# Optimization experiments

Measured on AMD Instinct MI355X. Metric: run time of the kernel, lower is better.

Reference implementation:

```python
import jax, jax.numpy as jnp
import numpy as np

B, S, D, H = 8, 2048, 1024, 8
CHUNK = D // H
SCALE = float(D) ** (-0.5)  # key_dim ** -0.5, key_dim == num_units here
LN_EPS = 1e-5


def setup_inputs() -> dict:
    key = jax.random.key(0)
    ks = jax.random.split(key, 9)
    s = 0.02
    return {
        "query": jax.random.normal(ks[0], (B, S, D), jnp.float32),
        "keys": jax.random.normal(ks[1], (B, S, D), jnp.float32),
        "Wq": jax.random.normal(ks[2], (D, D), jnp.float32) * s,  # torch Linear weight [out,in]
        "Wk": jax.random.normal(ks[3], (D, D), jnp.float32) * s,
        "Wv": jax.random.normal(ks[4], (D, D), jnp.float32) * s,
        "Wp": jax.random.normal(ks[5], (D, D), jnp.float32) * s,
        "bp": jnp.zeros((D,), jnp.float32),
        "ln_gamma": jnp.ones((D,), jnp.float32),
        "ln_beta": jnp.zeros((D,), jnp.float32),
    }


def reference(query, keys, Wq, Wk, Wv, Wp, bp, ln_gamma, ln_beta):
    # Linear layers (no bias on q/k/v): y = x @ W.T
    Q = jnp.einsum("bsd,ed->bse", query, Wq)
    K = jnp.einsum("bsd,ed->bse", keys, Wk)
    V = jnp.einsum("bsd,ed->bse", keys, Wv)
    # Faithful to original: raw view to [B*h, S, chunk] (no transpose head split)
    Qh = Q.reshape(B * H, S, CHUNK)
    Kh = K.reshape(B * H, S, CHUNK)
    Vh = V.reshape(B * H, S, CHUNK)
    # scores [B*h, S, S], scale, softmax (is_masked=False, dropout_p=0)
    att = jnp.einsum("gqc,gkc->gqk", Qh, Kh) * SCALE
    att = jax.nn.softmax(att, axis=-1)
    ctx = jnp.einsum("gqk,gkc->gqc", att, Vh).reshape(B, S, D)
    # output projection + residual + LayerNorm
    out = jnp.einsum("bsd,ed->bse", ctx, Wp) + bp
    out = out + query
    mu = jnp.mean(out, axis=-1, keepdims=True)
    var = jnp.mean(jnp.square(out - mu), axis=-1, keepdims=True)
    out = (out - mu) * jax.lax.rsqrt(var + LN_EPS) * ln_gamma + ln_beta
    return out
```

## Files before the change

kernel.cpp:

```cpp
#include <hip/hip_runtime.h>

typedef __bf16 bf16x8 __attribute__((ext_vector_type(8)));
typedef float f32x4 __attribute__((ext_vector_type(4)));

#define SCLOG 0.04508422f

__device__ __forceinline__ unsigned short f2bf(float f) {
  union { float f; unsigned int u; } v;
  v.f = f;
  unsigned int u = v.u;
  u += 0x7fffu + ((u >> 16) & 1u);
  return (unsigned short)(u >> 16);
}

__device__ __forceinline__ void gld_lds16(const void* g, void* l) {
  __builtin_amdgcn_global_load_lds(
      (const __attribute__((address_space(1))) void*)g,
      (__attribute__((address_space(3))) void*)l, 16, 0, 0);
}

__global__ __launch_bounds__(256) void convert_kernel(
    const float* __restrict__ q, const float* __restrict__ k,
    const float* __restrict__ wq, const float* __restrict__ wk,
    const float* __restrict__ wv, const float* __restrict__ wp,
    unsigned short* __restrict__ qb, unsigned short* __restrict__ kb,
    unsigned short* __restrict__ Wqkv, unsigned short* __restrict__ Wpb) {
  size_t i = (size_t)blockIdx.x * 256 + threadIdx.x;
  const float* src; unsigned short* dst; size_t off;
  if (i < 4194304)      { src = q;  dst = qb;             off = i; }
  else if (i < 8388608) { src = k;  dst = kb;             off = i - 4194304; }
  else if (i < 8650752) { src = wq; dst = Wqkv;           off = i - 8388608; }
  else if (i < 8912896) { src = wk; dst = Wqkv + 1048576; off = i - 8650752; }
  else if (i < 9175040) { src = wv; dst = Wqkv + 2097152; off = i - 8912896; }
  else                  { src = wp; dst = Wpb;            off = i - 9175040; }
  float4 v = ((const float4*)src)[off];
  ushort4 o;
  o.x = f2bf(v.x); o.y = f2bf(v.y); o.z = f2bf(v.z); o.w = f2bf(v.w);
  ((ushort4*)dst)[off] = o;
}

#define QKV_BAR __builtin_amdgcn_s_barrier()
#define QKV_LGKM asm volatile("s_waitcnt lgkmcnt(0)" ::: "memory")

#define QKV_STG(lc, h, srcb, s)                                               \
  gld_lds16((srcb) + (size_t)(s) * 128 + gro0, (lc) + (h) * 16384 + d0);      \
  gld_lds16((srcb) + (size_t)(s) * 128 + gro1, (lc) + (h) * 16384 + d0 + 1024);

#define QKV_RDA(I0)                                                           \
  _Pragma("unroll") for (int i4 = 0; i4 < 4; ++i4) {                          \
    af[i4][0] = *(const bf16x8*)(tb + rbA + ((I0) + i4) * 2048 + cx0);        \
    af[i4][1] = *(const bf16x8*)(tb + rbA + ((I0) + i4) * 2048 + cx1);        \
  }

#define QKV_RDB(JP)                                                           \
  _Pragma("unroll") for (int j2 = 0; j2 < 2; ++j2) {                          \
    bfr[JP][j2][0] = *(const bf16x8*)(tb + rbB + ((JP) * 2 + j2) * 2048 + cx0); \
    bfr[JP][j2][1] = *(const bf16x8*)(tb + rbB + ((JP) * 2 + j2) * 2048 + cx1); \
  }

#define QKV_MM(I0, JP)                                                        \
  _Pragma("unroll") for (int i4 = 0; i4 < 4; ++i4)                            \
  _Pragma("unroll") for (int j2 = 0; j2 < 2; ++j2)                            \
  _Pragma("unroll") for (int kk = 0; kk < 2; ++kk)                            \
    acc[(I0) + i4][(JP) * 2 + j2] = __builtin_amdgcn_mfma_f32_16x16x32_bf16(  \
        af[i4][kk], bfr[JP][j2][kk], acc[(I0) + i4][(JP) * 2 + j2], 0, 0, 0);

__global__ __launch_bounds__(512, 2) void gemm_qkv8_kernel(
    const unsigned short* __restrict__ qb,
    const unsigned short* __restrict__ kb,
    const unsigned short* __restrict__ W,
    unsigned short* __restrict__ Qo,
    unsigned short* __restrict__ Ko,
    unsigned short* __restrict__ Vo) {
  __shared__ char lds[131072];

  const int t = threadIdx.x;
  const int lane = t & 63;
  const int w = t >> 6;
  const int fr = lane & 15;
  const int quad = lane >> 4;

  const int orig = blockIdx.x;
  const int sseq = orig >> 3;
  const int tn = sseq >> 3;
  const int tm = (orig & 7) * 8 + (sseq & 7);

  const unsigned short* Ap = (tn < 4) ? qb : kb;
  const char* aBase = (const char*)Ap + (size_t)(tm * 256) * 2048;
  const char* bBase = (const char*)W + (size_t)(tn * 256) * 2048;

  const int wm2 = w >> 2, wn4 = w & 3;

  const size_t gro0 = (size_t)(w * 16 + (lane >> 3)) * 2048 + (size_t)(((lane & 7) ^ (lane >> 3)) << 4);
  const size_t gro1 = gro0 + 8 * 2048;
  const int d0 = w * 2048 + lane * 16;

  const int rbA = (wm2 * 128 + fr) * 128;
  const int rbB = 32768 + (wn4 * 64 + fr) * 128;
  const int cx0 = (quad * 16) ^ ((fr & 7) << 4);
  const int cx1 = cx0 ^ 64;

  f32x4 acc[8][4];
#pragma unroll
  for (int i = 0; i < 8; ++i)
#pragma unroll
    for (int j = 0; j < 4; ++j) acc[i][j] = (f32x4){0.f, 0.f, 0.f, 0.f};

#pragma unroll
  for (int s = 0; s < 2; ++s) {
    char* lc = lds + s * 65536;
    QKV_STG(lc, 0, aBase, s);
    QKV_STG(lc, 1, aBase + 262144, s);
    QKV_STG(lc + 32768, 0, bBase, s);
    QKV_STG(lc + 32768, 1, bBase + 262144, s);
  }
  asm volatile("s_waitcnt vmcnt(8)" ::: "memory");
  QKV_BAR;

#pragma unroll 1
  for (int kt = 0; kt < 16; ++kt) {
    const char* tb = lds + (kt & 1) * 65536;
    char* lc = lds + (kt & 1) * 65536;
    const int s = kt + 2;
    bf16x8 af[4][2], bfr[2][2][2];

    QKV_RDA(0);
    QKV_RDB(0);
    QKV_BAR; QKV_LGKM;
    __builtin_amdgcn_s_setprio(1);
    QKV_MM(0, 0);
    __builtin_amdgcn_s_setprio(0);
    QKV_BAR;

    QKV_RDB(1);
    QKV_BAR; QKV_LGKM;
    __builtin_amdgcn_s_setprio(1);
    QKV_MM(0, 1);
    __builtin_amdgcn_s_setprio(0);
    QKV_BAR;

    QKV_RDA(4);
    if (s < 16) {
      QKV_STG(lc + 32768, 0, bBase, s);
      QKV_STG(lc + 32768, 1, bBase + 262144, s);
    }
    QKV_BAR; QKV_LGKM;
    __builtin_amdgcn_s_setprio(1);
    QKV_MM(4, 1);
    __builtin_amdgcn_s_setprio(0);
    QKV_BAR;

    if (s < 16) {
      QKV_STG(lc, 0, aBase, s);
      QKV_STG(lc, 1, aBase + 262144, s);
    }
    QKV_BAR;
    __builtin_amdgcn_s_setprio(1);
    QKV_MM(4, 0);
    __builtin_amdgcn_s_setprio(0);
    if (kt <= 13)      { asm volatile("s_waitcnt vmcnt(8)" ::: "memory"); }
    else if (kt == 14) { asm volatile("s_waitcnt vmcnt(0)" ::: "memory"); }
    if (kt < 15) QKV_BAR;
  }

  const int sel = tn >> 2;
  unsigned short* Out = sel == 0 ? Qo : (sel == 1 ? Ko : Vo);
  const float osc = (sel == 0) ? SCLOG : 1.f;
  const int row0 = tm * 256 + wm2 * 128 + quad * 4;
  const int col0 = (tn & 3) * 256 + wn4 * 64 + fr;
#pragma unroll
  for (int i = 0; i < 8; ++i)
#pragma unroll
    for (int j = 0; j < 4; ++j)
#pragma unroll
      for (int r = 0; r < 4; ++r)
        Out[(size_t)(row0 + i * 16 + r) * 1024 + col0 + j * 16] = f2bf(acc[i][j][r] * osc);
}

__global__ __launch_bounds__(256) void vtrans_kernel(
    const unsigned short* __restrict__ V, unsigned short* __restrict__ Vt) {
  __shared__ unsigned short T[128 * 136];
  const int g  = blockIdx.x >> 4;
  const int kt = blockIdx.x & 15;
  const unsigned short* Vg = V + (size_t)g * 262144 + (size_t)kt * 128 * 128;
  unsigned short* Vtg = Vt + (size_t)g * 262144 + kt * 128;
  const int t = threadIdx.x;
#pragma unroll
  for (int it = 0; it < 8; it++) {
    int seg = t + it * 256;
    int k  = seg >> 4;
    int c8 = (seg & 15) << 3;
    uint4 a = *(const uint4*)(Vg + k * 128 + c8);
    unsigned short* Tp = &T[c8 * 136 + k];
    Tp[0 * 136] = (unsigned short)(a.x & 0xffff);
    Tp[1 * 136] = (unsigned short)(a.x >> 16);
    Tp[2 * 136] = (unsigned short)(a.y & 0xffff);
    Tp[3 * 136] = (unsigned short)(a.y >> 16);
    Tp[4 * 136] = (unsigned short)(a.z & 0xffff);
    Tp[5 * 136] = (unsigned short)(a.z >> 16);
    Tp[6 * 136] = (unsigned short)(a.w & 0xffff);
    Tp[7 * 136] = (unsigned short)(a.w >> 16);
  }
  __syncthreads();
#pragma unroll
  for (int it = 0; it < 8; it++) {
    int seg = t + it * 256;
    int c  = seg >> 4;
    int k8 = (seg & 15) << 3;
    uint4 o = *(const uint4*)&T[c * 136 + k8];
    *(uint4*)(Vtg + (size_t)c * 2048 + k8) = o;
  }
}

#define ATTN_TILE(KSH, VSH, KST, VST, PREF)                                    \
  {                                                                            \
    if (PREF) {                                                                \
      gld_lds16(kp + kS0, (KST) + kD0);                                        \
      gld_lds16(kp + kS1, (KST) + kD1);                                        \
      gld_lds16(vp + vS0, (VST) + vD0);                                        \
      gld_lds16(vp + vS1, (VST) + vD1);                                        \
      kp += 8192; vp += 64;                                                    \
    }                                                                          \
    _Pragma("unroll")                                                          \
    for (int mt = 0; mt < 4; mt++) {                                           \
      bf16x8 kf[4];                                                            \
      _Pragma("unroll")                                                        \
      for (int kc = 0; kc < 4; kc++)                                           \
        kf[kc] = *(const bf16x8*)((KSH) + kfO[mt][kc]);                        \
      f32x4 s = (f32x4){0.f, 0.f, 0.f, 0.f};                                   \
      _Pragma("unroll")                                                        \
      for (int kc = 0; kc < 4; kc++)                                           \
        s = __builtin_amdgcn_mfma_f32_16x16x32_bf16(kf[kc], qf[kc], s, 0, 0, 0);\
      float e0 = __builtin_amdgcn_exp2f(fminf(s[0], 30.f));                    \
      float e1 = __builtin_amdgcn_exp2f(fminf(s[1], 30.f));                    \
      float e2 = __builtin_amdgcn_exp2f(fminf(s[2], 30.f));                    \
      float e3 = __builtin_amdgcn_exp2f(fminf(s[3], 30.f));                    \
      lp += (e0 + e1) + (e2 + e3);                                             \
      unsigned u01, u23;                                                       \
      asm("v_cvt_pk_bf16_f32 %0, %1, %2" : "=v"(u01) : "v"(e0), "v"(e1));      \
      asm("v_cvt_pk_bf16_f32 %0, %1, %2" : "=v"(u23) : "v"(e2), "v"(e3));      \
      uint2 u2; u2.x = u01; u2.y = u23;                                        \
      *(uint2*)(Psh + pWr[mt]) = u2;                                           \
    }                                                                          \
    {                                                                          \
      bf16x8 pf0 = *(const bf16x8*)(Psh + pRd0);                               \
      bf16x8 pf1 = *(const bf16x8*)(Psh + pRd1);                               \
      _Pragma("unroll")                                                        \
      for (int cb = 0; cb < 8; cb++) {                                         \
        O[cb] = __builtin_amdgcn_mfma_f32_16x16x32_bf16(                       \
            pf0, *(const bf16x8*)((VSH) + vfO[cb][0]), O[cb], 0, 0, 0);        \
        O[cb] = __builtin_amdgcn_mfma_f32_16x16x32_bf16(                       \
            pf1, *(const bf16x8*)((VSH) + vfO[cb][1]), O[cb], 0, 0, 0);        \
      }                                                                        \
    }                                                                          \
    __syncthreads();                                                           \
  }

__global__ __launch_bounds__(512, 4) void attn_kernel(
    const unsigned short* __restrict__ Q,
    const unsigned short* __restrict__ K,
    const unsigned short* __restrict__ Vt,
    unsigned short* __restrict__ ctx) {
  __shared__ unsigned char smem[81920];
  unsigned char* Psh = smem + 65536;

  const int g  = blockIdx.x >> 4;
  const int qt = blockIdx.x & 15;
  const unsigned short* Qg = Q + (size_t)g * 262144 + (size_t)qt * 16384;
  const unsigned short* Kg = K + (size_t)g * 262144;
  const unsigned short* Vg = Vt + (size_t)g * 262144;

  const int t    = threadIdx.x;
  const int lane = t & 63;
  const int wv   = t >> 6;
  const int fr   = lane & 15;
  const int quad = lane >> 4;
  const int qrow = wv * 16 + fr;

  int kfO[4][4];
#pragma unroll
  for (int mt = 0; mt < 4; mt++)
#pragma unroll
    for (int kc = 0; kc < 4; kc++) {
      int row = mt * 16 + fr;
      int c = kc * 4 + quad;
      int p = (c & 8) | ((c ^ (row & 7)) & 7);
      kfO[mt][kc] = row * 256 + p * 16;
    }
  int vfO[8][2];
#pragma unroll
  for (int cb = 0; cb < 8; cb++)
#pragma unroll
    for (int k2 = 0; k2 < 2; k2++) {
      int crow = cb * 16 + fr;
      int c = k2 * 4 + quad;
      int p = c ^ (crow & 7);
      vfO[cb][k2] = crow * 128 + p * 16;
    }
  int pWr[4];
#pragma unroll
  for (int mt = 0; mt < 4; mt++) {
    int cP = mt * 2 + (quad >> 1);
    int pP = cP ^ (qrow & 7);
    pWr[mt] = qrow * 128 + pP * 16 + (quad & 1) * 8;
  }
  int pRd0, pRd1;
  {
    int c0 = quad,     p0 = c0 ^ (qrow & 7);
    int c1 = 4 + quad, p1 = c1 ^ (qrow & 7);
    pRd0 = qrow * 128 + p0 * 16;
    pRd1 = qrow * 128 + p1 * 16;
  }
  int kS0, kS1, kD0, kD1, vS0, vS1, vD0, vD1;
  {
    int seg0 = t, seg1 = t + 512;
    int r0 = seg0 >> 4, p0 = seg0 & 15, c0 = (p0 & 8) | ((p0 ^ r0) & 7);
    int r1 = seg1 >> 4, p1 = seg1 & 15, c1 = (p1 & 8) | ((p1 ^ r1) & 7);
    kS0 = r0 * 128 + c0 * 8;  kD0 = seg0 * 16;
    kS1 = r1 * 128 + c1 * 8;  kD1 = seg1 * 16;
    int vr0 = seg0 >> 3, vp0 = seg0 & 7, vc0 = vp0 ^ (vr0 & 7);
    int vr1 = seg1 >> 3, vp1 = seg1 & 7, vc1 = vp1 ^ (vr1 & 7);
    vS0 = vr0 * 2048 + vc0 * 8;  vD0 = seg0 * 16;
    vS1 = vr1 * 2048 + vc1 * 8;  vD1 = seg1 * 16;
  }

#pragma unroll
  for (int it = 0; it < 4; it++) {
    int seg = t + it * 512;
    int r = seg >> 4, p = seg & 15;
    int c = (p & 8) | ((p ^ r) & 7);
    gld_lds16(Qg + r * 128 + c * 8, smem + seg * 16);
  }
  __syncthreads();
  bf16x8 qf[4];
#pragma unroll
  for (int kc = 0; kc < 4; kc++) {
    int c = kc * 4 + quad;
    int p = (c & 8) | ((c ^ (qrow & 7)) & 7);
    qf[kc] = *(const bf16x8*)(smem + qrow * 256 + p * 16);
  }
  __syncthreads();

  gld_lds16(Kg + kS0, smem + kD0);
  gld_lds16(Kg + kS1, smem + kD1);
  gld_lds16(Vg + vS0, smem + 32768 + vD0);
  gld_lds16(Vg + vS1, smem + 32768 + vD1);
  __syncthreads();

  const unsigned short* kp = Kg + 8192;
  const unsigned short* vp = Vg + 64;

  f32x4 O[8];
#pragma unroll
  for (int cb = 0; cb < 8; cb++) O[cb] = (f32x4){0.f, 0.f, 0.f, 0.f};
  float lp = 0.f;

  unsigned char* B0K = smem;
  unsigned char* B1K = smem + 16384;
  unsigned char* B0V = smem + 32768;
  unsigned char* B1V = smem + 49152;

#pragma unroll 1
  for (int kt2 = 0; kt2 < 16; kt2++) {
    ATTN_TILE(B0K, B0V, B1K, B1V, 1);
    ATTN_TILE(B1K, B1V, B0K, B0V, (kt2 < 15));
  }

  float* linv_arr = (float*)(smem + 65536);
  {
    float v = lp;
    v += __shfl_xor(v, 16);
    v += __shfl_xor(v, 32);
    if (quad == 0) linv_arr[wv * 16 + fr] = 1.f / v;
  }
  unsigned short* Cg = ctx + (size_t)g * 262144 + (size_t)qt * 16384;
  float li[4];
#pragma unroll
  for (int r = 0; r < 4; r++) li[r] = linv_arr[wv * 16 + quad * 4 + r];
#pragma unroll
  for (int cb = 0; cb < 8; cb++)
#pragma unroll
    for (int r = 0; r < 4; r++) {
      int orow = wv * 16 + quad * 4 + r;
      Cg[(size_t)orow * 128 + cb * 16 + fr] = f2bf(O[cb][r] * li[r]);
    }
}

__global__ __launch_bounds__(256) void gemm_proj_kernel(
    const unsigned short* __restrict__ A,
    const unsigned short* __restrict__ W,
    const float* __restrict__ bp,
    const float* __restrict__ qres,
    float* __restrict__ out) {
  __shared__ unsigned short Alds[128 * 32];
  __shared__ unsigned short Blds[128 * 32];
  const int t   = threadIdx.x;
  const int bid = blockIdx.x;
  const int tn  = bid % 8;
  const int tm  = bid / 8;
  const unsigned short* Bptr = W + (size_t)tn * 128 * 1024;

  const int lane = t & 63;
  const int wv   = t >> 6;
  const int wm   = (wv >> 1) * 64;
  const int wn   = (wv & 1) * 64;
  const int fr   = lane & 15;
  const int kq   = (lane >> 4) * 8;

  f32x4 acc[4][4];
#pragma unroll
  for (int i = 0; i < 4; i++)
#pragma unroll
    for (int j = 0; j < 4; j++) acc[i][j] = (f32x4){0.f, 0.f, 0.f, 0.f};

  const int sr = t >> 2;
  const int sc = (t & 3) << 3;
  const unsigned short* gA = A + (size_t)(tm * 128 + sr) * 1024 + sc;
  const unsigned short* gB = Bptr + (size_t)sr * 1024 + sc;
  unsigned short* lA = Alds + t * 8;
  unsigned short* lB = Blds + t * 8;

  for (int k0 = 0; k0 < 1024; k0 += 32) {
    gld_lds16(gA, lA);
    gld_lds16(gA + 64 * 1024, lA + 64 * 32);
    gld_lds16(gB, lB);
    gld_lds16(gB + 64 * 1024, lB + 64 * 32);
    gA += 32; gB += 32;
    __syncthreads();
    bf16x8 af[4], bfr[4];
#pragma unroll
    for (int i = 0; i < 4; i++) {
      af[i]  = *(const bf16x8*)&Alds[(wm + i * 16 + fr) * 32 + kq];
      bfr[i] = *(const bf16x8*)&Blds[(wn + i * 16 + fr) * 32 + kq];
    }
#pragma unroll
    for (int i = 0; i < 4; i++)
#pragma unroll
      for (int j = 0; j < 4; j++)
        acc[i][j] = __builtin_amdgcn_mfma_f32_16x16x32_bf16(af[i], bfr[j], acc[i][j], 0, 0, 0);
    __syncthreads();
  }

  const int quad = lane >> 4;
  const int cc   = lane & 15;
#pragma unroll
  for (int i = 0; i < 4; i++)
#pragma unroll
    for (int j = 0; j < 4; j++)
#pragma unroll
      for (int r = 0; r < 4; r++) {
        int row = tm * 128 + wm + i * 16 + quad * 4 + r;
        int col = tn * 128 + wn + j * 16 + cc;
        out[(size_t)row * 1024 + col] =
            acc[i][j][r] + bp[col] + qres[(size_t)row * 1024 + col];
      }
}

__global__ __launch_bounds__(256) void ln_kernel(float* __restrict__ out,
                                                 const float* __restrict__ gamma,
                                                 const float* __restrict__ beta) {
  __shared__ float red[8];
  const int row = blockIdx.x;
  float* p = out + (size_t)row * 1024;
  const int t = threadIdx.x;
  float4 v = ((const float4*)p)[t];
  float s  = v.x + v.y + v.z + v.w;
  float s2 = v.x * v.x + v.y * v.y + v.z * v.z + v.w * v.w;
#pragma unroll
  for (int off = 1; off < 64; off <<= 1) {
    s  += __shfl_xor(s, off);
    s2 += __shfl_xor(s2, off);
  }
  const int wv = t >> 6;
  if ((t & 63) == 0) { red[wv] = s; red[4 + wv] = s2; }
  __syncthreads();
  float S  = red[0] + red[1] + red[2] + red[3];
  float S2 = red[4] + red[5] + red[6] + red[7];
  float mu  = S * (1.f / 1024.f);
  float var = S2 * (1.f / 1024.f) - mu * mu;
  float rstd = rsqrtf(var + 1e-5f);
  float4 gm = ((const float4*)gamma)[t];
  float4 bt = ((const float4*)beta)[t];
  v.x = (v.x - mu) * rstd * gm.x + bt.x;
  v.y = (v.y - mu) * rstd * gm.y + bt.y;
  v.z = (v.z - mu) * rstd * gm.z + bt.z;
  v.w = (v.w - mu) * rstd * gm.w + bt.w;
  ((float4*)p)[t] = v;
}

extern "C" void kernel_launch(void* const* d_in, const int* in_sizes, int n_in,
                              void* d_out, int out_size, void* d_ws, size_t ws_size,
                              hipStream_t stream) {
  const float* query = (const float*)d_in[0];
  const float* keys  = (const float*)d_in[1];
  const float* Wq    = (const float*)d_in[2];
  const float* Wk    = (const float*)d_in[3];
  const float* Wv    = (const float*)d_in[4];
  const float* Wp    = (const float*)d_in[5];
  const float* bp    = (const float*)d_in[6];
  const float* gamma = (const float*)d_in[7];
  const float* beta  = (const float*)d_in[8];
  float* out = (float*)d_out;

  unsigned short* ws   = (unsigned short*)d_ws;
  unsigned short* qb   = ws;
  unsigned short* kb   = ws + 16777216;
  unsigned short* Wqkv = ws + 33554432;
  unsigned short* Wpb  = ws + 36700160;
  unsigned short* Qb   = ws + 37748736;
  unsigned short* Kb   = ws + 54525952;
  unsigned short* Vb   = ws + 71303168;
  unsigned short* Vtb  = kb;
  unsigned short* ctx  = qb;

  convert_kernel<<<36864, 256, 0, stream>>>(query, keys, Wq, Wk, Wv, Wp, qb, kb, Wqkv, Wpb);
  gemm_qkv8_kernel<<<768, 512, 0, stream>>>(qb, kb, Wqkv, Qb, Kb, Vb);
  vtrans_kernel<<<1024, 256, 0, stream>>>(Vb, Vtb);
  attn_kernel<<<1024, 512, 0, stream>>>(Qb, Kb, Vtb, ctx);
  gemm_proj_kernel<<<1024, 256, 0, stream>>>(ctx, Wpb, bp, query, out);
  ln_kernel<<<16384, 256, 0, stream>>>(out, gamma, beta);
}
```

Before: 542.7 us.

## Switch attention to 32x32x16 MFMA with register P via permlane32 swap

```diff
diff --git a/kernel.cpp b/kernel.cpp
--- a/kernel.cpp
+++ b/kernel.cpp
@@ -2,6 +2,8 @@
 
 typedef __bf16 bf16x8 __attribute__((ext_vector_type(8)));
 typedef float f32x4 __attribute__((ext_vector_type(4)));
+typedef float f32x16 __attribute__((ext_vector_type(16)));
+typedef unsigned uint2e __attribute__((ext_vector_type(2)));
 
 #define SCLOG 0.04508422f
 
@@ -212,6 +214,21 @@
   }
 }
 
+#define PACK_HALF(EX, KSBASE)                                                  \
+    _Pragma("unroll")                                                          \
+    for (int c2 = 0; c2 < 2; c2++)                                             \
+      _Pragma("unroll")                                                        \
+      for (int e = 0; e < 2; e++) {                                            \
+        unsigned ua, ub;                                                       \
+        asm("v_cvt_pk_bf16_f32 %0, %1, %2" : "=v"(ua)                          \
+            : "v"(EX[8 * c2 + 2 * e]), "v"(EX[8 * c2 + 2 * e + 1]));           \
+        asm("v_cvt_pk_bf16_f32 %0, %1, %2" : "=v"(ub)                          \
+            : "v"(EX[8 * c2 + 4 + 2 * e]), "v"(EX[8 * c2 + 4 + 2 * e + 1]));   \
+        uint2e rr = __builtin_amdgcn_permlane32_swap(ua, ub, false, false);    \
+        if (e == 0) { paw[(KSBASE) + c2].x = rr[0]; paw[(KSBASE) + c2].z = rr[1]; } \
+        else        { paw[(KSBASE) + c2].y = rr[0]; paw[(KSBASE) + c2].w = rr[1]; } \
+      }
+
 #define ATTN_TILE(KSH, VSH, KST, VST, PREF)                                    \
   {                                                                            \
     if (PREF) {                                                                \
@@ -221,36 +238,44 @@
       gld_lds16(vp + vS1, (VST) + vD1);                                        \
       kp += 8192; vp += 64;                                                    \
     }                                                                          \
+    f32x16 s0, s1;                                                             \
     _Pragma("unroll")                                                          \
-    for (int mt = 0; mt < 4; mt++) {                                           \
-      bf16x8 kf[4];                                                            \
+    for (int r = 0; r < 16; r++) { s0[r] = 0.f; s1[r] = 0.f; }                 \
+    {                                                                          \
+      bf16x8 kf[8];                                                            \
       _Pragma("unroll")                                                        \
-      for (int kc = 0; kc < 4; kc++)                                           \
-        kf[kc] = *(const bf16x8*)((KSH) + kfO[mt][kc]);                        \
-      f32x4 s = (f32x4){0.f, 0.f, 0.f, 0.f};                                   \
+      for (int ks = 0; ks < 8; ks++)                                           \
+        kf[ks] = *(const bf16x8*)((KSH) + kb0 + kOf[ks]);                      \
       _Pragma("unroll")                                                        \
-      for (int kc = 0; kc < 4; kc++)                                           \
-        s = __builtin_amdgcn_mfma_f32_16x16x32_bf16(kf[kc], qf[kc], s, 0, 0, 0);\
-      float e0 = __builtin_amdgcn_exp2f(fminf(s[0], 30.f));                    \
-      float e1 = __builtin_amdgcn_exp2f(fminf(s[1], 30.f));                    \
-      float e2 = __builtin_amdgcn_exp2f(fminf(s[2], 30.f));                    \
-      float e3 = __builtin_amdgcn_exp2f(fminf(s[3], 30.f));                    \
-      lp += (e0 + e1) + (e2 + e3);                                             \
-      unsigned u01, u23;                                                       \
-      asm("v_cvt_pk_bf16_f32 %0, %1, %2" : "=v"(u01) : "v"(e0), "v"(e1));      \
-      asm("v_cvt_pk_bf16_f32 %0, %1, %2" : "=v"(u23) : "v"(e2), "v"(e3));      \
-      uint2 u2; u2.x = u01; u2.y = u23;                                        \
-      *(uint2*)(Psh + pWr[mt]) = u2;                                           \
+      for (int ks = 0; ks < 8; ks++)                                           \
+        s0 = __builtin_amdgcn_mfma_f32_32x32x16_bf16(kf[ks], qf[ks], s0, 0, 0, 0); \
     }                                                                          \
     {                                                                          \
-      bf16x8 pf0 = *(const bf16x8*)(Psh + pRd0);                               \
-      bf16x8 pf1 = *(const bf16x8*)(Psh + pRd1);                               \
+      bf16x8 kf[8];                                                            \
       _Pragma("unroll")                                                        \
-      for (int cb = 0; cb < 8; cb++) {                                         \
-        O[cb] = __builtin_amdgcn_mfma_f32_16x16x32_bf16(                       \
-            pf0, *(const bf16x8*)((VSH) + vfO[cb][0]), O[cb], 0, 0, 0);        \
-        O[cb] = __builtin_amdgcn_mfma_f32_16x16x32_bf16(                       \
-            pf1, *(const bf16x8*)((VSH) + vfO[cb][1]), O[cb], 0, 0, 0);        \
+      for (int ks = 0; ks < 8; ks++)                                           \
+        kf[ks] = *(const bf16x8*)((KSH) + kb0 + 8192 + kOf[ks]);               \
+      _Pragma("unroll")                                                        \
+      for (int ks = 0; ks < 8; ks++)                                           \
+        s1 = __builtin_amdgcn_mfma_f32_32x32x16_bf16(kf[ks], qf[ks], s1, 0, 0, 0); \
+    }                                                                          \
+    float ex0[16], ex1[16];                                                    \
+    _Pragma("unroll")                                                          \
+    for (int r = 0; r < 16; r++) {                                             \
+      ex0[r] = __builtin_amdgcn_exp2f(fminf(s0[r], 30.f));                     \
+      ex1[r] = __builtin_amdgcn_exp2f(fminf(s1[r], 30.f));                     \
+      lp += ex0[r] + ex1[r];                                                   \
+    }                                                                          \
+    uint4 paw[4];                                                              \
+    PACK_HALF(ex0, 0)                                                          \
+    PACK_HALF(ex1, 2)                                                          \
+    _Pragma("unroll")                                                          \
+    for (int cb = 0; cb < 4; cb++) {                                           \
+      _Pragma("unroll")                                                        \
+      for (int ks = 0; ks < 4; ks++) {                                         \
+        bf16x8 vf = *(const bf16x8*)((VSH) + cb * 4096 + vOf[ks]);             \
+        bf16x8 pa8 = __builtin_bit_cast(bf16x8, paw[ks]);                      \
+        O[cb] = __builtin_amdgcn_mfma_f32_32x32x16_bf16(pa8, vf, O[cb], 0, 0, 0); \
       }                                                                        \
     }                                                                          \
     __syncthreads();                                                           \
@@ -261,55 +286,34 @@
     const unsigned short* __restrict__ K,
     const unsigned short* __restrict__ Vt,
     unsigned short* __restrict__ ctx) {
-  __shared__ unsigned char smem[81920];
-  unsigned char* Psh = smem + 65536;
-
-  const int g  = blockIdx.x >> 4;
-  const int qt = blockIdx.x & 15;
-  const unsigned short* Qg = Q + (size_t)g * 262144 + (size_t)qt * 16384;
+  __shared__ unsigned char smem[65536];
+
+  const int bid = blockIdx.x;
+  const int g  = (bid & 7) * 8 + (bid >> 6);
+  const int qt = (bid >> 3) & 7;
+  const unsigned short* Qg = Q + (size_t)g * 262144 + (size_t)qt * 32768;
   const unsigned short* Kg = K + (size_t)g * 262144;
   const unsigned short* Vg = Vt + (size_t)g * 262144;
 
   const int t    = threadIdx.x;
   const int lane = t & 63;
   const int wv   = t >> 6;
-  const int fr   = lane & 15;
-  const int quad = lane >> 4;
-  const int qrow = wv * 16 + fr;
-
-  int kfO[4][4];
-#pragma unroll
-  for (int mt = 0; mt < 4; mt++)
-#pragma unroll
-    for (int kc = 0; kc < 4; kc++) {
-      int row = mt * 16 + fr;
-      int c = kc * 4 + quad;
-      int p = (c & 8) | ((c ^ (row & 7)) & 7);
-      kfO[mt][kc] = row * 256 + p * 16;
-    }
-  int vfO[8][2];
-#pragma unroll
-  for (int cb = 0; cb < 8; cb++)
-#pragma unroll
-    for (int k2 = 0; k2 < 2; k2++) {
-      int crow = cb * 16 + fr;
-      int c = k2 * 4 + quad;
-      int p = c ^ (crow & 7);
-      vfO[cb][k2] = crow * 128 + p * 16;
-    }
-  int pWr[4];
-#pragma unroll
-  for (int mt = 0; mt < 4; mt++) {
-    int cP = mt * 2 + (quad >> 1);
-    int pP = cP ^ (qrow & 7);
-    pWr[mt] = qrow * 128 + pP * 16 + (quad & 1) * 8;
-  }
-  int pRd0, pRd1;
-  {
-    int c0 = quad,     p0 = c0 ^ (qrow & 7);
-    int c1 = 4 + quad, p1 = c1 ^ (qrow & 7);
-    pRd0 = qrow * 128 + p0 * 16;
-    pRd1 = qrow * 128 + p1 * 16;
+  const int col  = lane & 31;
+  const int hi   = lane >> 5;
+  const int qrow = wv * 32 + col;
+
+  int kOf[8];
+#pragma unroll
+  for (int ks = 0; ks < 8; ks++) {
+    int c = ks * 2 + hi;
+    kOf[ks] = ((c & 8) | ((c ^ (col & 7)) & 7)) << 4;
+  }
+  const int kb0 = col * 256;
+  int vOf[4];
+#pragma unroll
+  for (int ks = 0; ks < 4; ks++) {
+    int c = ks * 2 + hi;
+    vOf[ks] = col * 128 + (((c ^ (col & 7)) & 7) << 4);
   }
   int kS0, kS1, kD0, kD1, vS0, vS1, vD0, vD1;
   {
@@ -325,19 +329,19 @@
   }
 
 #pragma unroll
-  for (int it = 0; it < 4; it++) {
+  for (int it = 0; it < 8; it++) {
     int seg = t + it * 512;
     int r = seg >> 4, p = seg & 15;
     int c = (p & 8) | ((p ^ r) & 7);
     gld_lds16(Qg + r * 128 + c * 8, smem + seg * 16);
   }
   __syncthreads();
-  bf16x8 qf[4];
-#pragma unroll
-  for (int kc = 0; kc < 4; kc++) {
-    int c = kc * 4 + quad;
+  bf16x8 qf[8];
+#pragma unroll
+  for (int ks = 0; ks < 8; ks++) {
+    int c = ks * 2 + hi;
     int p = (c & 8) | ((c ^ (qrow & 7)) & 7);
-    qf[kc] = *(const bf16x8*)(smem + qrow * 256 + p * 16);
+    qf[ks] = *(const bf16x8*)(smem + qrow * 256 + p * 16);
   }
   __syncthreads();
 
@@ -350,9 +354,11 @@
   const unsigned short* kp = Kg + 8192;
   const unsigned short* vp = Vg + 64;
 
-  f32x4 O[8];
-#pragma unroll
-  for (int cb = 0; cb < 8; cb++) O[cb] = (f32x4){0.f, 0.f, 0.f, 0.f};
+  f32x16 O[4];
+#pragma unroll
+  for (int cb = 0; cb < 4; cb++)
+#pragma unroll
+    for (int r = 0; r < 16; r++) O[cb][r] = 0.f;
   float lp = 0.f;
 
   unsigned char* B0K = smem;
@@ -366,24 +372,24 @@
     ATTN_TILE(B1K, B1V, B0K, B0V, (kt2 < 15));
   }
 
-  float* linv_arr = (float*)(smem + 65536);
-  {
-    float v = lp;
-    v += __shfl_xor(v, 16);
-    v += __shfl_xor(v, 32);
-    if (quad == 0) linv_arr[wv * 16 + fr] = 1.f / v;
-  }
-  unsigned short* Cg = ctx + (size_t)g * 262144 + (size_t)qt * 16384;
-  float li[4];
-#pragma unroll
-  for (int r = 0; r < 4; r++) li[r] = linv_arr[wv * 16 + quad * 4 + r];
-#pragma unroll
-  for (int cb = 0; cb < 8; cb++)
-#pragma unroll
-    for (int r = 0; r < 4; r++) {
-      int orow = wv * 16 + quad * 4 + r;
-      Cg[(size_t)orow * 128 + cb * 16 + fr] = f2bf(O[cb][r] * li[r]);
-    }
+  lp += __shfl_xor(lp, 32);
+  float* linv_arr = (float*)smem;
+  linv_arr[wv * 32 + col] = 1.f / lp;
+  float4 li[4];
+#pragma unroll
+  for (int rq = 0; rq < 4; rq++)
+    li[rq] = *(const float4*)&linv_arr[wv * 32 + rq * 8 + hi * 4];
+
+  unsigned short* Cg = ctx + (size_t)g * 262144 + (size_t)qt * 32768;
+#pragma unroll
+  for (int cb = 0; cb < 4; cb++)
+#pragma unroll
+    for (int rq = 0; rq < 4; rq++)
+#pragma unroll
+      for (int j = 0; j < 4; j++) {
+        int row = wv * 32 + rq * 8 + hi * 4 + j;
+        Cg[(size_t)row * 128 + cb * 32 + col] = f2bf(O[cb][rq * 4 + j] * li[rq][j]);
+      }
 }
 
 __global__ __launch_bounds__(256) void gemm_proj_kernel(
@@ -516,7 +522,7 @@
   convert_kernel<<<36864, 256, 0, stream>>>(query, keys, Wq, Wk, Wv, Wp, qb, kb, Wqkv, Wpb);
   gemm_qkv8_kernel<<<768, 512, 0, stream>>>(qb, kb, Wqkv, Qb, Kb, Vb);
   vtrans_kernel<<<1024, 256, 0, stream>>>(Vb, Vtb);
-  attn_kernel<<<1024, 512, 0, stream>>>(Qb, Kb, Vtb, ctx);
+  attn_kernel<<<512, 512, 0, stream>>>(Qb, Kb, Vtb, ctx);
   gemm_proj_kernel<<<1024, 256, 0, stream>>>(ctx, Wpb, bp, query, out);
   ln_kernel<<<16384, 256, 0, stream>>>(out, gamma, beta);
 }
```

Result: slower. 913.4 us (+68.3%).
